# Performance work log

Hardware: AMD Instinct MI355X
Metric: run time of the kernel (lower is better)

Reference implementation:

```python
import jax, jax.numpy as jnp
import numpy as np

DIM = 64
NUM_HEADS = 2
HEAD_DIM = DIM // NUM_HEADS


def setup_inputs() -> dict:
    key = jax.random.key(0)
    k1, k2, k3 = jax.random.split(key, 3)
    b, c, h, w = 8, DIM, 256, 256
    x = jax.random.normal(k1, (b, c, h, w), dtype=jnp.float32)
    # 1x1 conv weights, stored as [out_ch, in_ch] (kernel spatial dims are 1)
    qkv_w = jax.random.normal(k2, (3 * c, c), dtype=jnp.float32) * (1.0 / np.sqrt(c))
    proj_w = jax.random.normal(k3, (c, c), dtype=jnp.float32) * (1.0 / np.sqrt(c))
    return {"x": x, "qkv_w": qkv_w, "proj_w": proj_w}


def _phi(t):
    # elu(x) + 1 feature map (positive-valued kernel features)
    return jax.nn.elu(t) + 1.0


def reference(x, qkv_w, proj_w):
    b, c, h, w = x.shape
    n = h * w
    # 1x1 conv == per-pixel channel matmul
    qkv = jnp.einsum('oc,bchw->bohw', qkv_w, x)  # [b, 3c, h, w]
    q, k, v = jnp.split(qkv, 3, axis=1)

    def reshape(t):
        return t.reshape(b, NUM_HEADS, HEAD_DIM, n)  # bhcn

    q_phi = _phi(reshape(q))
    k_phi = _phi(reshape(k))
    v_h = reshape(v)
    # KV outer product over the sequence dim: tiny [b, h, c, d]
    KV = jnp.einsum('bhcn,bhdn->bhcd', k_phi, v_h)
    out_h = jnp.einsum('bhcn,bhcd->bhdn', q_phi, KV)  # [b, h, d, n]
    out = out_h.reshape(b, c, h, w)
    return jnp.einsum('oc,bchw->bohw', proj_w, out)
```

## Files before the change

kernel.cpp:

```cpp
#include <hip/hip_runtime.h>
#include <hip/hip_bf16.h>

#define BATCH 8
#define CH    64
#define NPIX  65536
#define NHEAD 2
#define HDIM  32

typedef __attribute__((ext_vector_type(8))) short bf16x8;
typedef __attribute__((ext_vector_type(4))) float f32x4;

#define MFMA(a, b, c) __builtin_amdgcn_mfma_f32_16x16x32_bf16(a, b, c, 0, 0, 0)

__device__ __forceinline__ unsigned rne_pk(float lo, float hi) {
    unsigned ua = __float_as_uint(lo); ua += 0x7fffu + ((ua >> 16) & 1u);
    unsigned ub = __float_as_uint(hi); ub += 0x7fffu + ((ub >> 16) & 1u);
    return (ua >> 16) | (ub & 0xffff0000u);
}

__device__ __forceinline__ bf16x8 pack8(const float* f) {
    int4 iv;
    iv.x = (int)rne_pk(f[0], f[1]);
    iv.y = (int)rne_pk(f[2], f[3]);
    iv.z = (int)rne_pk(f[4], f[5]);
    iv.w = (int)rne_pk(f[6], f[7]);
    return *reinterpret_cast<bf16x8*>(&iv);
}

__device__ __forceinline__ float phi_f(float t) {
    return t > 0.0f ? t + 1.0f : __expf(t);
}

__device__ __forceinline__ bf16x8 load_w_frag(const float* W, int r0, int k0, int lane) {
    const float* p = W + (size_t)(r0 + (lane & 15)) * 64 + k0 + ((lane >> 4) << 3);
    float f[8];
    #pragma unroll
    for (int e = 0; e < 8; e++) f[e] = p[e];
    return pack8(f);
}

__global__ __launch_bounds__(256) void la_pass1(
    const float* __restrict__ x, const float* __restrict__ qkv_w,
    float* __restrict__ kv)
{
    __shared__ __align__(16) unsigned char smem[40960];

    const int tid  = threadIdx.x;
    const int lane = tid & 63;
    const int wv   = __builtin_amdgcn_readfirstlane(tid >> 6);
    const int b    = blockIdx.y;
    const int g    = lane >> 4;
    const int li   = lane & 15;

    unsigned short* kls = (unsigned short*)(smem + wv * 10240);
    unsigned short* vls = kls + 64 * 40;

    bf16x8 Wf[8][2];
    #pragma unroll
    for (int j = 0; j < 8; j++)
        #pragma unroll
        for (int ks = 0; ks < 2; ks++)
            Wf[j][ks] = load_w_frag(qkv_w, 64 + 16 * j, 32 * ks, lane);

    f32x4 kvacc[2][2][2];
    #pragma unroll
    for (int h = 0; h < 2; h++)
        #pragma unroll
        for (int mt = 0; mt < 2; mt++)
            #pragma unroll
            for (int nt = 0; nt < 2; nt++)
                kvacc[h][mt][nt] = (f32x4){0.f, 0.f, 0.f, 0.f};

    const float* xb = x + (size_t)b * CH * NPIX;

    for (int s = blockIdx.x * 4 + wv; s < 2048; s += 256) {
        const int px0 = s * 32;

        bf16x8 xa[2][2];
        #pragma unroll
        for (int mt = 0; mt < 2; mt++) {
            const float* xp = xb + px0 + 16 * mt + li;
            #pragma unroll
            for (int ks = 0; ks < 2; ks++) {
                float f[8];
                #pragma unroll
                for (int e = 0; e < 8; e++)
                    f[e] = xp[(size_t)(32 * ks + 8 * g + e) * NPIX];
                xa[mt][ks] = pack8(f);
            }
        }

        #pragma unroll
        for (int j = 0; j < 8; j++) {
            unsigned short* dst = (j < 4) ? kls : vls;
            const int crow = (j & 3) * 16 + li;
            #pragma unroll
            for (int mt = 0; mt < 2; mt++) {
                f32x4 acc = (f32x4){0.f, 0.f, 0.f, 0.f};
                acc = MFMA(xa[mt][0], Wf[j][0], acc);
                acc = MFMA(xa[mt][1], Wf[j][1], acc);
                float v0 = acc[0], v1 = acc[1], v2 = acc[2], v3 = acc[3];
                if (j < 4) { v0 = phi_f(v0); v1 = phi_f(v1); v2 = phi_f(v2); v3 = phi_f(v3); }
                *reinterpret_cast<uint2*>(dst + crow * 40 + 16 * mt + 4 * g) =
                    make_uint2(rne_pk(v0, v1), rne_pk(v2, v3));
            }
        }

        #pragma unroll
        for (int h = 0; h < 2; h++) {
            bf16x8 af[2], bv[2];
            #pragma unroll
            for (int mt = 0; mt < 2; mt++)
                af[mt] = *reinterpret_cast<const bf16x8*>(kls + (32 * h + 16 * mt + li) * 40 + 8 * g);
            #pragma unroll
            for (int nt = 0; nt < 2; nt++)
                bv[nt] = *reinterpret_cast<const bf16x8*>(vls + (32 * h + 16 * nt + li) * 40 + 8 * g);
            #pragma unroll
            for (int mt = 0; mt < 2; mt++)
                #pragma unroll
                for (int nt = 0; nt < 2; nt++)
                    kvacc[h][mt][nt] = MFMA(af[mt], bv[nt], kvacc[h][mt][nt]);
        }
    }

    __syncthreads();
    float* rbuf = (float*)smem;
    #pragma unroll
    for (int h = 0; h < 2; h++)
        #pragma unroll
        for (int mt = 0; mt < 2; mt++)
            #pragma unroll
            for (int nt = 0; nt < 2; nt++) {
                const int t = (h * 2 + mt) * 2 + nt;
                #pragma unroll
                for (int r = 0; r < 4; r++)
                    rbuf[wv * 2048 + t * 256 + (4 * g + r) * 16 + li] = kvacc[h][mt][nt][r];
            }
    __syncthreads();

    float* kvb = kv + (size_t)b * NHEAD * HDIM * HDIM;
    for (int i = 0; i < 8; i++) {
        const int idx = i * 256 + tid;
        const float sum = rbuf[idx] + rbuf[2048 + idx] + rbuf[4096 + idx] + rbuf[6144 + idx];
        const int t = idx >> 8, within = idx & 255;
        const int row = within >> 4, col = within & 15;
        const int h = t >> 2, mt = (t >> 1) & 1, nt = t & 1;
        atomicAdd(&kvb[(h * 32 + 16 * mt + row) * 32 + 16 * nt + col], sum);
    }
}

__global__ __launch_bounds__(256) void la_pass2(
    const float* __restrict__ x, const float* __restrict__ qkv_w,
    const float* __restrict__ proj_w, const float* __restrict__ kv,
    float* __restrict__ y)
{
    __shared__ __align__(16) unsigned short sm2[4][2][16][72];

    const int tid  = threadIdx.x;
    const int lane = tid & 63;
    const int wv   = __builtin_amdgcn_readfirstlane(tid >> 6);
    const int b    = blockIdx.y;
    const int g    = lane >> 4;
    const int li   = lane & 15;

    unsigned short* qT = &sm2[wv][0][0][0];
    unsigned short* oT = &sm2[wv][1][0][0];

    bf16x8 Aq[4][2], Ap[4][2], Akv[2][2];
    #pragma unroll
    for (int mt = 0; mt < 4; mt++)
        #pragma unroll
        for (int ks = 0; ks < 2; ks++) {
            Aq[mt][ks] = load_w_frag(qkv_w, 16 * mt, 32 * ks, lane);
            Ap[mt][ks] = load_w_frag(proj_w, 16 * mt, 32 * ks, lane);
        }
    const float* kvb = kv + (size_t)b * NHEAD * HDIM * HDIM;
    #pragma unroll
    for (int h = 0; h < 2; h++)
        #pragma unroll
        for (int mtd = 0; mtd < 2; mtd++) {
            float f[8];
            #pragma unroll
            for (int e = 0; e < 8; e++)
                f[e] = kvb[h * 1024 + (8 * g + e) * 32 + 16 * mtd + li];
            Akv[h][mtd] = pack8(f);
        }

    const float* xb = x + (size_t)b * CH * NPIX;
    float*       yb = y + (size_t)b * CH * NPIX;

    for (int s = blockIdx.x * 4 + wv; s < 4096; s += 512) {
        const int px0 = s * 16;

        bf16x8 bx[2];
        const float* xp = xb + px0 + li;
        #pragma unroll
        for (int ks = 0; ks < 2; ks++) {
            float f[8];
            #pragma unroll
            for (int e = 0; e < 8; e++)
                f[e] = xp[(size_t)(32 * ks + 8 * g + e) * NPIX];
            bx[ks] = pack8(f);
        }

        #pragma unroll
        for (int mt = 0; mt < 4; mt++) {
            f32x4 acc = (f32x4){0.f, 0.f, 0.f, 0.f};
            acc = MFMA(Aq[mt][0], bx[0], acc);
            acc = MFMA(Aq[mt][1], bx[1], acc);
            const float p0 = phi_f(acc[0]), p1 = phi_f(acc[1]);
            const float p2 = phi_f(acc[2]), p3 = phi_f(acc[3]);
            *reinterpret_cast<uint2*>(qT + li * 72 + 16 * mt + 4 * g) =
                make_uint2(rne_pk(p0, p1), rne_pk(p2, p3));
        }

        #pragma unroll
        for (int h = 0; h < 2; h++) {
            const bf16x8 bq = *reinterpret_cast<const bf16x8*>(qT + li * 72 + 32 * h + 8 * g);
            #pragma unroll
            for (int mtd = 0; mtd < 2; mtd++) {
                f32x4 acc = (f32x4){0.f, 0.f, 0.f, 0.f};
                acc = MFMA(Akv[h][mtd], bq, acc);
                *reinterpret_cast<uint2*>(oT + li * 72 + 32 * h + 16 * mtd + 4 * g) =
                    make_uint2(rne_pk(acc[0], acc[1]), rne_pk(acc[2], acc[3]));
            }
        }

        const bf16x8 bo0 = *reinterpret_cast<const bf16x8*>(oT + li * 72 + 8 * g);
        const bf16x8 bo1 = *reinterpret_cast<const bf16x8*>(oT + li * 72 + 32 + 8 * g);
        #pragma unroll
        for (int mt = 0; mt < 4; mt++) {
            f32x4 acc = (f32x4){0.f, 0.f, 0.f, 0.f};
            acc = MFMA(Ap[mt][0], bo0, acc);
            acc = MFMA(Ap[mt][1], bo1, acc);
            #pragma unroll
            for (int r = 0; r < 4; r++)
                yb[(size_t)(16 * mt + 4 * g + r) * NPIX + px0 + li] = acc[r];
        }
    }
}

extern "C" void kernel_launch(void* const* d_in, const int* in_sizes, int n_in,
                              void* d_out, int out_size, void* d_ws, size_t ws_size,
                              hipStream_t stream) {
    (void)in_sizes; (void)n_in; (void)out_size; (void)ws_size;
    const float* x      = (const float*)d_in[0];
    const float* qkv_w  = (const float*)d_in[1];
    const float* proj_w = (const float*)d_in[2];
    float* yout = (float*)d_out;
    float* kv   = (float*)d_ws;

    hipMemsetAsync(kv, 0, (size_t)BATCH * NHEAD * HDIM * HDIM * sizeof(float), stream);

    la_pass1<<<dim3(64, BATCH), dim3(256), 0, stream>>>(x, qkv_w, kv);
    la_pass2<<<dim3(128, BATCH), dim3(256), 0, stream>>>(x, qkv_w, proj_w, kv, yout);
}
```

Before: 106.2 us.

## Replace pass1 atomics with per-block partials and a separate reduce kernel

Pass1 now writes each block's KV partial sum to its own workspace slot instead of issuing atomicAdd into a zeroed buffer. A new small kernel sums the partials per batch, which also removes the memset. The pass1 grid is halved, so each wave processes more pixel strips. This trades atomic contention and the memset for an extra kernel launch and fewer resident blocks during the memory-bound pass.

```diff
diff --git a/kernel.cpp b/kernel.cpp
--- a/kernel.cpp
+++ b/kernel.cpp
@@ -6,6 +6,7 @@
 #define NPIX  65536
 #define NHEAD 2
 #define HDIM  32
+#define P1_BLOCKS 32
 
 typedef __attribute__((ext_vector_type(8))) short bf16x8;
 typedef __attribute__((ext_vector_type(4))) float f32x4;
@@ -41,7 +42,7 @@
 
 __global__ __launch_bounds__(256) void la_pass1(
     const float* __restrict__ x, const float* __restrict__ qkv_w,
-    float* __restrict__ kv)
+    float* __restrict__ partials)
 {
     __shared__ __align__(16) unsigned char smem[40960];
 
@@ -73,7 +74,7 @@
 
     const float* xb = x + (size_t)b * CH * NPIX;
 
-    for (int s = blockIdx.x * 4 + wv; s < 2048; s += 256) {
+    for (int s = blockIdx.x * 4 + wv; s < 2048; s += P1_BLOCKS * 4) {
         const int px0 = s * 32;
 
         bf16x8 xa[2][2];
@@ -138,14 +139,28 @@
             }
     __syncthreads();
 
-    float* kvb = kv + (size_t)b * NHEAD * HDIM * HDIM;
+    float* outp = partials + ((size_t)b * P1_BLOCKS + blockIdx.x) * 2048;
     for (int i = 0; i < 8; i++) {
         const int idx = i * 256 + tid;
         const float sum = rbuf[idx] + rbuf[2048 + idx] + rbuf[4096 + idx] + rbuf[6144 + idx];
         const int t = idx >> 8, within = idx & 255;
         const int row = within >> 4, col = within & 15;
         const int h = t >> 2, mt = (t >> 1) & 1, nt = t & 1;
-        atomicAdd(&kvb[(h * 32 + 16 * mt + row) * 32 + 16 * nt + col], sum);
+        outp[(h * 32 + 16 * mt + row) * 32 + 16 * nt + col] = sum;
+    }
+}
+
+__global__ __launch_bounds__(256) void la_reduce(
+    const float* __restrict__ partials, float* __restrict__ kv)
+{
+    const int b = blockIdx.x;
+    const int t = threadIdx.x;
+    for (int e = t; e < 2048; e += 256) {
+        const float* p = partials + (size_t)b * P1_BLOCKS * 2048 + e;
+        float s = 0.0f;
+        #pragma unroll
+        for (int j = 0; j < P1_BLOCKS; j++) s += p[(size_t)j * 2048];
+        kv[(size_t)b * 2048 + e] = s;
     }
 }
 
@@ -248,10 +263,11 @@
     const float* qkv_w  = (const float*)d_in[1];
     const float* proj_w = (const float*)d_in[2];
     float* yout = (float*)d_out;
-    float* kv   = (float*)d_ws;
-
-    hipMemsetAsync(kv, 0, (size_t)BATCH * NHEAD * HDIM * HDIM * sizeof(float), stream);
-
-    la_pass1<<<dim3(64, BATCH), dim3(256), 0, stream>>>(x, qkv_w, kv);
-    la_pass2<<<dim3(128, BATCH), dim3(256), 0, stream>>>(x, qkv_w, proj_w, kv, yout);
-}
+
+    float* partials = (float*)d_ws;
+    float* kv       = partials + (size_t)BATCH * P1_BLOCKS * 2048;
+
+    la_pass1 <<<dim3(P1_BLOCKS, BATCH), dim3(256), 0, stream>>>(x, qkv_w, partials);
+    la_reduce<<<dim3(BATCH),            dim3(256), 0, stream>>>(partials, kv);
+    la_pass2 <<<dim3(128, BATCH),       dim3(256), 0, stream>>>(x, qkv_w, proj_w, kv, yout);
+}
```

Result: slower. 119.2 us (+12.3%).
